# Performance work log

Measured on AMD Instinct MI355X. Metric: run time of the kernel, lower is better.

## Reference

```python
import jax, jax.numpy as jnp
import numpy as np

NUM_HEADS = 16
ROPE_BASE = 10000.0
MAX_POS = 4096


def _rope_tables(head_dim):
    inv_freq = 1.0 / (ROPE_BASE ** (np.arange(0, head_dim, 2, dtype=np.float32) / head_dim))
    freqs = np.arange(MAX_POS, dtype=np.float32)[:, None] * inv_freq[None, :]
    emb = np.concatenate([freqs, freqs], axis=-1)  # [MAX_POS, head_dim]
    return jnp.asarray(np.cos(emb)), jnp.asarray(np.sin(emb))


def _rotate_half(x):
    d = x.shape[-1] // 2
    return jnp.concatenate([-x[..., d:], x[..., :d]], axis=-1)


def _apply_rope(x, pos, cos_t, sin_t):
    # x: [B,H,S,D], pos: [B,S]
    cos = cos_t[pos][:, None]  # [B,1,S,D]
    sin = sin_t[pos][:, None]
    return x * cos + _rotate_half(x) * sin


def setup_inputs() -> dict:
    key = jax.random.key(0)
    ks = jax.random.split(key, 8)
    B, N, M, C = 2, 2048, 2048, 1024
    s = 1.0 / np.sqrt(C)
    return {
        "query": jax.random.normal(ks[0], (B, N, C), jnp.float32),
        "key": jax.random.normal(ks[1], (B, M, C), jnp.float32),
        "query_pos": jnp.broadcast_to(jnp.arange(N, dtype=jnp.int32), (B, N)),
        "key_pos": jnp.broadcast_to(jnp.arange(M, dtype=jnp.int32), (B, M)),
        "Wq": jax.random.normal(ks[2], (C, C), jnp.float32) * s,
        "bq": jnp.zeros((C,), jnp.float32),
        "Wk": jax.random.normal(ks[3], (C, C), jnp.float32) * s,
        "Wv": jax.random.normal(ks[4], (C, C), jnp.float32) * s,
        "bv": jnp.zeros((C,), jnp.float32),
        "Wo": jax.random.normal(ks[5], (C, C), jnp.float32) * s,
        "bo": jnp.zeros((C,), jnp.float32),
    }


def reference(query, key, query_pos, key_pos, Wq, bq, Wk, Wv, bv, Wo, bo):
    B, N, C = query.shape
    M = key.shape[1]
    H = NUM_HEADS
    D = C // H
    scale = D ** -0.5
    cos_t, sin_t = _rope_tables(D)

    value = key  # value defaults to key
    identity = query

    q = (query @ Wq.T + bq).reshape(B, N, H, D).transpose(0, 2, 1, 3)
    k = (key @ Wk.T).reshape(B, M, H, D).transpose(0, 2, 1, 3)
    v = (value @ Wv.T + bv).reshape(B, M, H, D).transpose(0, 2, 1, 3)

    q = _apply_rope(q, query_pos, cos_t, sin_t)
    k = _apply_rope(k, key_pos, cos_t, sin_t)

    attn = jnp.einsum('bhnd,bhmd->bhnm', q, k) * scale
    attn = jax.nn.softmax(attn, axis=-1)
    x = jnp.einsum('bhnm,bhmd->bhnd', attn, v)  # [B,H,N,D]
    x = x.transpose(0, 2, 1, 3).reshape(B, N, C)
    x = x @ Wo.T + bo
    return x + identity
```

## Files before the change

### kernel.cpp

```cpp
#include <hip/hip_runtime.h>
#include <hip/hip_bf16.h>
#include <stdint.h>

#define B_ 2
#define N_ 2048
#define M_ 2048
#define C_ 1024
#define H_ 16
#define D_ 64

typedef __attribute__((ext_vector_type(8))) short s16x8;
typedef __attribute__((ext_vector_type(4))) short s16x4;
typedef __attribute__((ext_vector_type(4))) float f32x4;
typedef __attribute__((ext_vector_type(16))) float f32x16;

__device__ __attribute__((always_inline)) inline short f2b(float f){
    __hip_bfloat16 h = __float2bfloat16(f); short s; __builtin_memcpy(&s, &h, 2); return s;
}
__device__ __attribute__((always_inline)) inline float b2f(short s){
    __hip_bfloat16 h; __builtin_memcpy(&h, &s, 2); return __bfloat162float(h);
}

#define MFMA16(a,b,c) __builtin_amdgcn_mfma_f32_16x16x32_bf16(a,b,c,0,0,0)
#define MFMA32(a,b,c) __builtin_amdgcn_mfma_f32_32x32x16_bf16(a,b,c,0,0,0)

__device__ __attribute__((always_inline)) inline void gl_lds16(const void* g, void* l){
    __builtin_amdgcn_global_load_lds((__attribute__((address_space(1))) void*)g,
                                     (__attribute__((address_space(3))) void*)l, 16, 0, 0);
}
__device__ __attribute__((always_inline)) inline unsigned fbits(float f){
    unsigned u; __builtin_memcpy(&u, &f, 4); return u;
}

__global__ void cvt_all(const float* __restrict__ q, const float* __restrict__ k,
                        const float* __restrict__ wq, const float* __restrict__ wk,
                        const float* __restrict__ wv, const float* __restrict__ wo,
                        short* __restrict__ dst){
    long i = ((long)blockIdx.x * 256 + threadIdx.x) * 8;
    const float* src; long off;
    if      (i <  4194304L){ src = q;  off = i; }
    else if (i <  8388608L){ src = k;  off = i - 4194304L; }
    else if (i <  9437184L){ src = wq; off = i - 8388608L; }
    else if (i < 10485760L){ src = wk; off = i - 9437184L; }
    else if (i < 11534336L){ src = wv; off = i - 10485760L; }
    else                   { src = wo; off = i - 11534336L; }
    float4 a = *(const float4*)(src + off);
    float4 b = *(const float4*)(src + off + 4);
    s16x8 o;
    o[0]=f2b(a.x); o[1]=f2b(a.y); o[2]=f2b(a.z); o[3]=f2b(a.w);
    o[4]=f2b(b.x); o[5]=f2b(b.y); o[6]=f2b(b.z); o[7]=f2b(b.w);
    *(s16x8*)(dst + i) = o;
}

__global__ __launch_bounds__(256, 2) void gemm_qkv(
    const short* __restrict__ qbf, const short* __restrict__ kbf,
    const short* __restrict__ W,
    const float* __restrict__ bq, const float* __restrict__ bv,
    short* __restrict__ qproj, short* __restrict__ kproj, short* __restrict__ vproj)
{
    __shared__ short As[128 * 32];
    __shared__ short Bs[128 * 32];
    const int n0 = blockIdx.x * 128, m0 = blockIdx.y * 128;
    const int sel = n0 >> 10;
    const short* A = (sel == 0) ? qbf : kbf;
    const int tid = threadIdx.x, lane = tid & 63, wave = tid >> 6;
    const int quad = lane >> 4, l16 = lane & 15;
    const int wr = (wave >> 1) * 64, wc = (wave & 1) * 64;
    const int srow = lane >> 2, scol = (lane & 3) * 8;

    f32x4 acc[4][4] = {};

    const short* Ag = A + (size_t)(m0 + wave * 32 + srow) * C_ + scol;
    const short* Bg = W + (size_t)(n0 + wave * 32 + srow) * C_ + scol;
    short* lA0 = As + (wave * 32) * 32;
    short* lA1 = As + (wave * 32 + 16) * 32;
    short* lB0 = Bs + (wave * 32) * 32;
    short* lB1 = Bs + (wave * 32 + 16) * 32;

    for (int k0 = 0; k0 < C_; k0 += 32){
        __syncthreads();
        gl_lds16(Ag + k0, lA0);
        gl_lds16(Ag + k0 + 16 * (size_t)C_, lA1);
        gl_lds16(Bg + k0, lB0);
        gl_lds16(Bg + k0 + 16 * (size_t)C_, lB1);
        __syncthreads();
        s16x8 af[4], bfr[4];
        #pragma unroll
        for (int t = 0; t < 4; t++) af[t]  = *(const s16x8*)&As[(wr + t*16 + l16) * 32 + quad * 8];
        #pragma unroll
        for (int t = 0; t < 4; t++) bfr[t] = *(const s16x8*)&Bs[(wc + t*16 + l16) * 32 + quad * 8];
        #pragma unroll
        for (int i = 0; i < 4; i++)
            #pragma unroll
            for (int j = 0; j < 4; j++)
                acc[i][j] = MFMA16(af[i], bfr[j], acc[i][j]);
    }

    short* dst = (sel == 0) ? qproj : ((sel == 1) ? kproj : vproj);
    const float* bp = (sel == 0) ? bq : ((sel == 2) ? bv : nullptr);
    const int coff = sel << 10;
    #pragma unroll
    for (int j = 0; j < 4; j++){
        int c = n0 + wc + j * 16 + l16 - coff;
        float bb = bp ? bp[c] : 0.0f;
        #pragma unroll
        for (int i = 0; i < 4; i++){
            int row = m0 + wr + i * 16 + quad * 4;
            #pragma unroll
            for (int r = 0; r < 4; r++)
                dst[(size_t)(row + r) * C_ + c] = f2b(acc[i][j][r] + bb);
        }
    }
}

__global__ __launch_bounds__(256, 2) void gemm_out(
    const short* __restrict__ A, const short* __restrict__ W,
    const float* __restrict__ bias, const float* __restrict__ resid,
    float* __restrict__ outf)
{
    __shared__ short As[128 * 32];
    __shared__ short Bs[128 * 32];
    const int n0 = blockIdx.x * 128, m0 = blockIdx.y * 128;
    const int tid = threadIdx.x, lane = tid & 63, wave = tid >> 6;
    const int quad = lane >> 4, l16 = lane & 15;
    const int wr = (wave >> 1) * 64, wc = (wave & 1) * 64;
    const int srow = lane >> 2, scol = (lane & 3) * 8;

    f32x4 acc[4][4] = {};
    const short* Ag = A + (size_t)(m0 + wave * 32 + srow) * C_ + scol;
    const short* Bg = W + (size_t)(n0 + wave * 32 + srow) * C_ + scol;
    short* lA0 = As + (wave * 32) * 32;
    short* lA1 = As + (wave * 32 + 16) * 32;
    short* lB0 = Bs + (wave * 32) * 32;
    short* lB1 = Bs + (wave * 32 + 16) * 32;

    for (int k0 = 0; k0 < C_; k0 += 32){
        __syncthreads();
        gl_lds16(Ag + k0, lA0);
        gl_lds16(Ag + k0 + 16 * (size_t)C_, lA1);
        gl_lds16(Bg + k0, lB0);
        gl_lds16(Bg + k0 + 16 * (size_t)C_, lB1);
        __syncthreads();
        s16x8 af[4], bfr[4];
        #pragma unroll
        for (int t = 0; t < 4; t++) af[t]  = *(const s16x8*)&As[(wr + t*16 + l16) * 32 + quad * 8];
        #pragma unroll
        for (int t = 0; t < 4; t++) bfr[t] = *(const s16x8*)&Bs[(wc + t*16 + l16) * 32 + quad * 8];
        #pragma unroll
        for (int i = 0; i < 4; i++)
            #pragma unroll
            for (int j = 0; j < 4; j++)
                acc[i][j] = MFMA16(af[i], bfr[j], acc[i][j]);
    }

    #pragma unroll
    for (int j = 0; j < 4; j++){
        int c = n0 + wc + j * 16 + l16;
        float bb = bias[c];
        #pragma unroll
        for (int i = 0; i < 4; i++){
            int row = m0 + wr + i * 16 + quad * 4;
            #pragma unroll
            for (int r = 0; r < 4; r++){
                size_t idx = (size_t)(row + r) * C_ + c;
                outf[idx] = acc[i][j][r] + bb + resid[idx];
            }
        }
    }
}

__global__ void rope_kernel(short* __restrict__ q, short* __restrict__ k,
                            const int* __restrict__ qpos, const int* __restrict__ kpos){
    const int QP = B_ * N_ * H_ * 32;
    int idx = blockIdx.x * blockDim.x + threadIdx.x;
    if (idx >= 2 * QP) return;
    bool isK = idx >= QP;
    int t = isK ? idx - QP : idx;
    int i = t & 31;
    int h = (t >> 5) & (H_ - 1);
    int row = t >> 9;
    int pos = isK ? kpos[row] : qpos[row];
    short* base = (isK ? k : q) + (size_t)row * C_ + h * D_;
    float x1 = b2f(base[i]), x2 = b2f(base[i + 32]);
    float invf = exp2f((float)i * (-13.287712379549449f / 32.0f));
    float f = (float)pos * invf;
    float c = cosf(f), s = sinf(f);
    float o1 = x1 * c - x2 * s;
    float o2 = x2 * c + x1 * s;
    float fac = isK ? 1.0f : (0.125f * 1.4426950408889634f);
    base[i]      = f2b(o1 * fac);
    base[i + 32] = f2b(o2 * fac);
}

__global__ void transpose_v(const short* __restrict__ v, short* __restrict__ vt){
    __shared__ short tile[64][72];
    int b = blockIdx.y >> 4, h = blockIdx.y & 15, mt = blockIdx.x;
    int tid = threadIdx.x;
    for (int c = tid; c < 512; c += 256){
        int m = c >> 3, d8 = (c & 7) * 8;
        *(s16x8*)&tile[m][d8] =
            *(const s16x8*)&v[((size_t)(b * M_ + mt * 64 + m)) * C_ + h * D_ + d8];
    }
    __syncthreads();
    for (int c = tid; c < 512; c += 256){
        int d = c >> 3, m8 = (c & 7) * 8;
        s16x8 o;
        #pragma unroll
        for (int jj = 0; jj < 8; jj++) o[jj] = tile[m8 + jj][d];
        *(s16x8*)&vt[(((size_t)(b * H_ + h)) * D_ + d) * M_ + mt * 64 + m8] = o;
    }
}

__global__ __launch_bounds__(256, 2) void flash_attn(
    const short* __restrict__ q, const short* __restrict__ k,
    const short* __restrict__ vt, short* __restrict__ o)
{
    __shared__ short smem[27136];
    const int b = blockIdx.y >> 4, h = blockIdx.y & 15;
    const int n0 = blockIdx.x * 128;
    const int tid = threadIdx.x, lane = tid & 63, wave = tid >> 6;
    const int hi = lane >> 5, l32 = lane & 31;
    const int wq = wave & 1, kq = wave >> 1;

    s16x8 qf[2][4];
    #pragma unroll
    for (int qt = 0; qt < 2; qt++)
        #pragma unroll
        for (int c = 0; c < 4; c++)
            qf[qt][c] = *(const s16x8*)&q[((size_t)(b * N_ + n0 + wq * 64 + qt * 32 + l32)) * C_
                                          + h * D_ + c * 16 + hi * 8];

    const short* kg = k  + (size_t)(b * M_) * C_ + h * D_;
    const short* vg = vt + ((size_t)(b * H_ + h)) * D_ * M_;
    const int srow0 = tid >> 3, sseg = (tid & 7) * 8;

    union V8 { s16x8 v; uint2 u[2]; };
    V8 kreg[2], vreg[2];

    #pragma unroll
    for (int ii = 0; ii < 2; ii++){
        int row = srow0 + 32 * ii;
        kreg[ii].v = *(const s16x8*)&kg[(size_t)row * C_ + sseg];
        vreg[ii].v = *(const s16x8*)&vg[(size_t)row * M_ + sseg];
    }
    #pragma unroll
    for (int ii = 0; ii < 2; ii++){
        int row = srow0 + 32 * ii;
        short* kd = &smem[row * 68 + sseg];
        *(uint2*)kd = kreg[ii].u[0]; *(uint2*)(kd + 4) = kreg[ii].u[1];
        short* vd = &smem[8704 + row * 68 + sseg];
        *(uint2*)vd = vreg[ii].u[0]; *(uint2*)(vd + 4) = vreg[ii].u[1];
    }

    f32x16 zero16 = {};
    f32x16 oacc[2][2] = {zero16, zero16, zero16, zero16};
    float lacc[2] = {0.f, 0.f};
    short* Pw = &smem[17408 + wave * 2304];

    for (int st = 0; st < 32; st++){
        const int p = st & 1;
        __syncthreads();
        if (st < 31){
            #pragma unroll
            for (int ii = 0; ii < 2; ii++){
                int row = srow0 + 32 * ii;
                kreg[ii].v = *(const s16x8*)&kg[((size_t)((st + 1) * 64 + row)) * C_ + sseg];
                vreg[ii].v = *(const s16x8*)&vg[(size_t)row * M_ + (st + 1) * 64 + sseg];
            }
        }
        const short* Kp = &smem[p * 4352];
        const short* Vp = &smem[8704 + p * 4352];

        s16x4 kf[4][2];
        #pragma unroll
        for (int c = 0; c < 4; c++){
            const short* a = &Kp[(kq * 32 + l32) * 68 + c * 16 + hi * 8];
            kf[c][0] = *(const s16x4*)a; kf[c][1] = *(const s16x4*)(a + 4);
        }
        #pragma unroll
        for (int qt = 0; qt < 2; qt++){
            f32x16 sv = {};
            #pragma unroll
            for (int c = 0; c < 4; c++){
                s16x8 ka = __builtin_shufflevector(kf[c][0], kf[c][1], 0,1,2,3,4,5,6,7);
                sv = MFMA32(ka, qf[qt][c], sv);
            }
            float ls = 0.f;
            unsigned pb[8];
            #pragma unroll
            for (int g = 0; g < 4; g++){
                float p0 = __builtin_amdgcn_exp2f(sv[4*g+0]);
                float p1 = __builtin_amdgcn_exp2f(sv[4*g+1]);
                float p2 = __builtin_amdgcn_exp2f(sv[4*g+2]);
                float p3 = __builtin_amdgcn_exp2f(sv[4*g+3]);
                ls += (p0 + p1) + (p2 + p3);
                pb[2*g]   = __builtin_amdgcn_perm(fbits(p1), fbits(p0), 0x07060302);
                pb[2*g+1] = __builtin_amdgcn_perm(fbits(p3), fbits(p2), 0x07060302);
            }
            lacc[qt] += ls;
            #pragma unroll
            for (int g = 0; g < 4; g++){
                short* d = &Pw[(qt * 32 + l32) * 36 + 8 * g + 4 * hi];
                uint2 u; u.x = pb[2*g]; u.y = pb[2*g+1];
                *(uint2*)d = u;
            }
        }
        asm volatile("s_waitcnt lgkmcnt(0)" ::: "memory");

        s16x8 pf[2][2], vf[2][2];
        #pragma unroll
        for (int qt = 0; qt < 2; qt++)
            #pragma unroll
            for (int c = 0; c < 2; c++){
                const short* a = &Pw[(qt * 32 + l32) * 36 + c * 16 + hi * 8];
                pf[qt][c] = __builtin_shufflevector(*(const s16x4*)a, *(const s16x4*)(a + 4),
                                                    0,1,2,3,4,5,6,7);
            }
        #pragma unroll
        for (int dt = 0; dt < 2; dt++)
            #pragma unroll
            for (int c = 0; c < 2; c++){
                const short* a = &Vp[(dt * 32 + l32) * 68 + kq * 32 + c * 16 + hi * 8];
                vf[dt][c] = __builtin_shufflevector(*(const s16x4*)a, *(const s16x4*)(a + 4),
                                                    0,1,2,3,4,5,6,7);
            }
        #pragma unroll
        for (int qt = 0; qt < 2; qt++)
            #pragma unroll
            for (int dt = 0; dt < 2; dt++)
                #pragma unroll
                for (int c = 0; c < 2; c++)
                    oacc[qt][dt] = MFMA32(pf[qt][c], vf[dt][c], oacc[qt][dt]);

        __syncthreads();
        if (st < 31){
            int pn = p ^ 1;
            #pragma unroll
            for (int ii = 0; ii < 2; ii++){
                int row = srow0 + 32 * ii;
                short* kd = &smem[pn * 4352 + row * 68 + sseg];
                *(uint2*)kd = kreg[ii].u[0]; *(uint2*)(kd + 4) = kreg[ii].u[1];
                short* vd = &smem[8704 + pn * 4352 + row * 68 + sseg];
                *(uint2*)vd = vreg[ii].u[0]; *(uint2*)(vd + 4) = vreg[ii].u[1];
            }
        }
    }

    __syncthreads();

    float* LO   = (float*)smem;
    float* Lsum = (float*)&smem[26624];
    float* Linv = Lsum + 128;

    float l0[2];
    #pragma unroll
    for (int qt = 0; qt < 2; qt++)
        l0[qt] = lacc[qt] + __shfl_xor(lacc[qt], 32);

    if (kq == 1){
        #pragma unroll
        for (int qt = 0; qt < 2; qt++)
            Lsum[wq * 64 + qt * 32 + l32] = l0[qt];
        #pragma unroll
        for (int qt = 0; qt < 2; qt++)
            #pragma unroll
            for (int dt = 0; dt < 2; dt++)
                #pragma unroll
                for (int e = 0; e < 16; e++){
                    int qrow = wq * 64 + qt * 32 + (e & 3) + 8 * (e >> 2) + 4 * hi;
                    LO[qrow * 65 + dt * 32 + l32] = oacc[qt][dt][e];
                }
    }
    __syncthreads();
    if (kq == 0){
        #pragma unroll
        for (int qt = 0; qt < 2; qt++){
            float lt = l0[qt] + Lsum[wq * 64 + qt * 32 + l32];
            Linv[wq * 64 + qt * 32 + l32] = 1.0f / lt;
        }
        asm volatile("s_waitcnt lgkmcnt(0)" ::: "memory");
        #pragma unroll
        for (int qt = 0; qt < 2; qt++)
            #pragma unroll
            for (int dt = 0; dt < 2; dt++)
                #pragma unroll
                for (int e = 0; e < 16; e++){
                    int qrow = wq * 64 + qt * 32 + (e & 3) + 8 * (e >> 2) + 4 * hi;
                    float val = (oacc[qt][dt][e] + LO[qrow * 65 + dt * 32 + l32]) * Linv[qrow];
                    o[((size_t)(b * N_ + n0 + qrow)) * C_ + h * D_ + dt * 32 + l32] = f2b(val);
                }
    }
}

extern "C" void kernel_launch(void* const* d_in, const int* in_sizes, int n_in,
                              void* d_out, int out_size, void* d_ws, size_t ws_size,
                              hipStream_t stream) {
    const float* query = (const float*)d_in[0];
    const float* key   = (const float*)d_in[1];
    const int*   qpos  = (const int*)d_in[2];
    const int*   kpos  = (const int*)d_in[3];
    const float* Wq    = (const float*)d_in[4];
    const float* bq    = (const float*)d_in[5];
    const float* Wk    = (const float*)d_in[6];
    const float* Wv    = (const float*)d_in[7];
    const float* bv    = (const float*)d_in[8];
    const float* Wo    = (const float*)d_in[9];
    const float* bo    = (const float*)d_in[10];
    float* out = (float*)d_out;

    const size_t E4M = (size_t)4 * 1024 * 1024;
    const size_t E1M = (size_t)1024 * 1024;
    short* ws    = (short*)d_ws;
    short* qbf   = ws;
    short* kbf   = qbf   + E4M;
    short* wqkvb = kbf   + E4M;
    short* wob   = wqkvb + 3 * E1M;
    short* qproj = wob   + E1M;
    short* kproj = qproj + E4M;
    short* vproj = kproj + E4M;
    short* vT    = qbf;
    short* attn  = kbf;

    cvt_all<<<6144, 256, 0, stream>>>(query, key, Wq, Wk, Wv, Wo, ws);

    gemm_qkv<<<dim3(24, 32), 256, 0, stream>>>(qbf, kbf, wqkvb, bq, bv,
                                               qproj, kproj, vproj);

    rope_kernel<<<(2 * B_ * N_ * H_ * 32) / 256, 256, 0, stream>>>(qproj, kproj, qpos, kpos);

    transpose_v<<<dim3(M_ / 64, B_ * H_), 256, 0, stream>>>(vproj, vT);

    flash_attn<<<dim3(16, 32), 256, 0, stream>>>(qproj, kproj, vT, attn);

    gemm_out<<<dim3(8, 32), 256, 0, stream>>>(attn, wob, bo, query, out);
}
```

Measured before the change: 235.5 us.

## Halve flash-attn and output-GEMM tiles to double block counts and raise occupancy

The flash attention kernel now handles 64 query rows per block instead of 128, doubling the grid to 1024 blocks, with a smaller shared-memory footprint and launch bounds raised to 3 blocks per CU. The output projection GEMM uses 128x64 tiles with each wave owning 32 rows, doubling its grid to 512 blocks at 4 blocks per CU. gemm_qkv's launch bound is also raised to 3. The goal is to fill the 256 CUs better than the earlier 512- and 256-block grids did. The cost is less K/V reuse per block, so more global and LDS traffic, and possible register spills under the tighter launch bounds.

```diff
diff --git a/kernel.cpp b/kernel.cpp
--- a/kernel.cpp
+++ b/kernel.cpp
@@ -52,7 +52,7 @@
     *(s16x8*)(dst + i) = o;
 }
 
-__global__ __launch_bounds__(256, 2) void gemm_qkv(
+__global__ __launch_bounds__(256, 3) void gemm_qkv(
     const short* __restrict__ qbf, const short* __restrict__ kbf,
     const short* __restrict__ W,
     const float* __restrict__ bq, const float* __restrict__ bv,
@@ -113,41 +113,39 @@
     }
 }
 
-__global__ __launch_bounds__(256, 2) void gemm_out(
+__global__ __launch_bounds__(256, 4) void gemm_out(
     const short* __restrict__ A, const short* __restrict__ W,
     const float* __restrict__ bias, const float* __restrict__ resid,
     float* __restrict__ outf)
 {
     __shared__ short As[128 * 32];
-    __shared__ short Bs[128 * 32];
-    const int n0 = blockIdx.x * 128, m0 = blockIdx.y * 128;
+    __shared__ short Bs[64 * 32];
+    const int n0 = blockIdx.x * 64, m0 = blockIdx.y * 128;
     const int tid = threadIdx.x, lane = tid & 63, wave = tid >> 6;
     const int quad = lane >> 4, l16 = lane & 15;
-    const int wr = (wave >> 1) * 64, wc = (wave & 1) * 64;
     const int srow = lane >> 2, scol = (lane & 3) * 8;
-
-    f32x4 acc[4][4] = {};
+    const int srowB = lane >> 2;
+
+    f32x4 acc[2][4] = {};
     const short* Ag = A + (size_t)(m0 + wave * 32 + srow) * C_ + scol;
-    const short* Bg = W + (size_t)(n0 + wave * 32 + srow) * C_ + scol;
+    const short* Bg = W + (size_t)(n0 + wave * 16 + srowB) * C_ + scol;
     short* lA0 = As + (wave * 32) * 32;
     short* lA1 = As + (wave * 32 + 16) * 32;
-    short* lB0 = Bs + (wave * 32) * 32;
-    short* lB1 = Bs + (wave * 32 + 16) * 32;
+    short* lB  = Bs + (wave * 16) * 32;
 
     for (int k0 = 0; k0 < C_; k0 += 32){
         __syncthreads();
         gl_lds16(Ag + k0, lA0);
         gl_lds16(Ag + k0 + 16 * (size_t)C_, lA1);
-        gl_lds16(Bg + k0, lB0);
-        gl_lds16(Bg + k0 + 16 * (size_t)C_, lB1);
-        __syncthreads();
-        s16x8 af[4], bfr[4];
-        #pragma unroll
-        for (int t = 0; t < 4; t++) af[t]  = *(const s16x8*)&As[(wr + t*16 + l16) * 32 + quad * 8];
-        #pragma unroll
-        for (int t = 0; t < 4; t++) bfr[t] = *(const s16x8*)&Bs[(wc + t*16 + l16) * 32 + quad * 8];
-        #pragma unroll
-        for (int i = 0; i < 4; i++)
+        gl_lds16(Bg + k0, lB);
+        __syncthreads();
+        s16x8 af[2], bfr[4];
+        #pragma unroll
+        for (int t = 0; t < 2; t++) af[t]  = *(const s16x8*)&As[(wave*32 + t*16 + l16) * 32 + quad * 8];
+        #pragma unroll
+        for (int t = 0; t < 4; t++) bfr[t] = *(const s16x8*)&Bs[(t*16 + l16) * 32 + quad * 8];
+        #pragma unroll
+        for (int i = 0; i < 2; i++)
             #pragma unroll
             for (int j = 0; j < 4; j++)
                 acc[i][j] = MFMA16(af[i], bfr[j], acc[i][j]);
@@ -155,11 +153,11 @@
 
     #pragma unroll
     for (int j = 0; j < 4; j++){
-        int c = n0 + wc + j * 16 + l16;
+        int c = n0 + j * 16 + l16;
         float bb = bias[c];
         #pragma unroll
-        for (int i = 0; i < 4; i++){
-            int row = m0 + wr + i * 16 + quad * 4;
+        for (int i = 0; i < 2; i++){
+            int row = m0 + wave * 32 + i * 16 + quad * 4;
             #pragma unroll
             for (int r = 0; r < 4; r++){
                 size_t idx = (size_t)(row + r) * C_ + c;
@@ -211,24 +209,22 @@
     }
 }
 
-__global__ __launch_bounds__(256, 2) void flash_attn(
+__global__ __launch_bounds__(256, 3) void flash_attn(
     const short* __restrict__ q, const short* __restrict__ k,
     const short* __restrict__ vt, short* __restrict__ o)
 {
-    __shared__ short smem[27136];
+    __shared__ short smem[22272];
     const int b = blockIdx.y >> 4, h = blockIdx.y & 15;
-    const int n0 = blockIdx.x * 128;
+    const int n0 = blockIdx.x * 64;
     const int tid = threadIdx.x, lane = tid & 63, wave = tid >> 6;
     const int hi = lane >> 5, l32 = lane & 31;
     const int wq = wave & 1, kq = wave >> 1;
 
-    s16x8 qf[2][4];
+    s16x8 qf[4];
     #pragma unroll
-    for (int qt = 0; qt < 2; qt++)
-        #pragma unroll
-        for (int c = 0; c < 4; c++)
-            qf[qt][c] = *(const s16x8*)&q[((size_t)(b * N_ + n0 + wq * 64 + qt * 32 + l32)) * C_
-                                          + h * D_ + c * 16 + hi * 8];
+    for (int c = 0; c < 4; c++)
+        qf[c] = *(const s16x8*)&q[((size_t)(b * N_ + n0 + wq * 32 + l32)) * C_
+                                  + h * D_ + c * 16 + hi * 8];
 
     const short* kg = k  + (size_t)(b * M_) * C_ + h * D_;
     const short* vg = vt + ((size_t)(b * H_ + h)) * D_ * M_;
@@ -253,9 +249,9 @@
     }
 
     f32x16 zero16 = {};
-    f32x16 oacc[2][2] = {zero16, zero16, zero16, zero16};
-    float lacc[2] = {0.f, 0.f};
-    short* Pw = &smem[17408 + wave * 2304];
+    f32x16 oacc[2] = {zero16, zero16};
+    float lacc = 0.f;
+    short* Pw = &smem[17408 + wave * 1152];
 
     for (int st = 0; st < 32; st++){
         const int p = st & 1;
@@ -277,45 +273,40 @@
             const short* a = &Kp[(kq * 32 + l32) * 68 + c * 16 + hi * 8];
             kf[c][0] = *(const s16x4*)a; kf[c][1] = *(const s16x4*)(a + 4);
         }
-        #pragma unroll
-        for (int qt = 0; qt < 2; qt++){
-            f32x16 sv = {};
-            #pragma unroll
-            for (int c = 0; c < 4; c++){
-                s16x8 ka = __builtin_shufflevector(kf[c][0], kf[c][1], 0,1,2,3,4,5,6,7);
-                sv = MFMA32(ka, qf[qt][c], sv);
-            }
-            float ls = 0.f;
-            unsigned pb[8];
-            #pragma unroll
-            for (int g = 0; g < 4; g++){
-                float p0 = __builtin_amdgcn_exp2f(sv[4*g+0]);
-                float p1 = __builtin_amdgcn_exp2f(sv[4*g+1]);
-                float p2 = __builtin_amdgcn_exp2f(sv[4*g+2]);
-                float p3 = __builtin_amdgcn_exp2f(sv[4*g+3]);
-                ls += (p0 + p1) + (p2 + p3);
-                pb[2*g]   = __builtin_amdgcn_perm(fbits(p1), fbits(p0), 0x07060302);
-                pb[2*g+1] = __builtin_amdgcn_perm(fbits(p3), fbits(p2), 0x07060302);
-            }
-            lacc[qt] += ls;
-            #pragma unroll
-            for (int g = 0; g < 4; g++){
-                short* d = &Pw[(qt * 32 + l32) * 36 + 8 * g + 4 * hi];
-                uint2 u; u.x = pb[2*g]; u.y = pb[2*g+1];
-                *(uint2*)d = u;
-            }
+        f32x16 sv = {};
+        #pragma unroll
+        for (int c = 0; c < 4; c++){
+            s16x8 ka = __builtin_shufflevector(kf[c][0], kf[c][1], 0,1,2,3,4,5,6,7);
+            sv = MFMA32(ka, qf[c], sv);
+        }
+        float ls = 0.f;
+        unsigned pb[8];
+        #pragma unroll
+        for (int g = 0; g < 4; g++){
+            float p0 = __builtin_amdgcn_exp2f(sv[4*g+0]);
+            float p1 = __builtin_amdgcn_exp2f(sv[4*g+1]);
+            float p2 = __builtin_amdgcn_exp2f(sv[4*g+2]);
+            float p3 = __builtin_amdgcn_exp2f(sv[4*g+3]);
+            ls += (p0 + p1) + (p2 + p3);
+            pb[2*g]   = __builtin_amdgcn_perm(fbits(p1), fbits(p0), 0x07060302);
+            pb[2*g+1] = __builtin_amdgcn_perm(fbits(p3), fbits(p2), 0x07060302);
+        }
+        lacc += ls;
+        #pragma unroll
+        for (int g = 0; g < 4; g++){
+            short* d = &Pw[l32 * 36 + 8 * g + 4 * hi];
+            uint2 u; u.x = pb[2*g]; u.y = pb[2*g+1];
+            *(uint2*)d = u;
         }
         asm volatile("s_waitcnt lgkmcnt(0)" ::: "memory");
 
-        s16x8 pf[2][2], vf[2][2];
-        #pragma unroll
-        for (int qt = 0; qt < 2; qt++)
-            #pragma unroll
-            for (int c = 0; c < 2; c++){
-                const short* a = &Pw[(qt * 32 + l32) * 36 + c * 16 + hi * 8];
-                pf[qt][c] = __builtin_shufflevector(*(const s16x4*)a, *(const s16x4*)(a + 4),
-                                                    0,1,2,3,4,5,6,7);
-            }
+        s16x8 pf[2], vf[2][2];
+        #pragma unroll
+        for (int c = 0; c < 2; c++){
+            const short* a = &Pw[l32 * 36 + c * 16 + hi * 8];
+            pf[c] = __builtin_shufflevector(*(const s16x4*)a, *(const s16x4*)(a + 4),
+                                            0,1,2,3,4,5,6,7);
+        }
         #pragma unroll
         for (int dt = 0; dt < 2; dt++)
             #pragma unroll
@@ -325,12 +316,10 @@
                                                     0,1,2,3,4,5,6,7);
             }
         #pragma unroll
-        for (int qt = 0; qt < 2; qt++)
-            #pragma unroll
-            for (int dt = 0; dt < 2; dt++)
-                #pragma unroll
-                for (int c = 0; c < 2; c++)
-                    oacc[qt][dt] = MFMA32(pf[qt][c], vf[dt][c], oacc[qt][dt]);
+        for (int dt = 0; dt < 2; dt++)
+            #pragma unroll
+            for (int c = 0; c < 2; c++)
+                oacc[dt] = MFMA32(pf[c], vf[dt][c], oacc[dt]);
 
         __syncthreads();
         if (st < 31){
@@ -349,46 +338,34 @@
     __syncthreads();
 
     float* LO   = (float*)smem;
-    float* Lsum = (float*)&smem[26624];
-    float* Linv = Lsum + 128;
-
-    float l0[2];
-    #pragma unroll
-    for (int qt = 0; qt < 2; qt++)
-        l0[qt] = lacc[qt] + __shfl_xor(lacc[qt], 32);
+    float* Lsum = (float*)&smem[22016];
+    float* Linv = Lsum + 64;
+
+    float l0 = lacc + __shfl_xor(lacc, 32);
 
     if (kq == 1){
-        #pragma unroll
-        for (int qt = 0; qt < 2; qt++)
-            Lsum[wq * 64 + qt * 32 + l32] = l0[qt];
-        #pragma unroll
-        for (int qt = 0; qt < 2; qt++)
-            #pragma unroll
-            for (int dt = 0; dt < 2; dt++)
-                #pragma unroll
-                for (int e = 0; e < 16; e++){
-                    int qrow = wq * 64 + qt * 32 + (e & 3) + 8 * (e >> 2) + 4 * hi;
-                    LO[qrow * 65 + dt * 32 + l32] = oacc[qt][dt][e];
-                }
+        Lsum[wq * 32 + l32] = l0;
+        #pragma unroll
+        for (int dt = 0; dt < 2; dt++)
+            #pragma unroll
+            for (int e = 0; e < 16; e++){
+                int qrow = wq * 32 + (e & 3) + 8 * (e >> 2) + 4 * hi;
+                LO[qrow * 65 + dt * 32 + l32] = oacc[dt][e];
+            }
     }
     __syncthreads();
     if (kq == 0){
-        #pragma unroll
-        for (int qt = 0; qt < 2; qt++){
-            float lt = l0[qt] + Lsum[wq * 64 + qt * 32 + l32];
-            Linv[wq * 64 + qt * 32 + l32] = 1.0f / lt;
-        }
+        float lt = l0 + Lsum[wq * 32 + l32];
+        Linv[wq * 32 + l32] = 1.0f / lt;
         asm volatile("s_waitcnt lgkmcnt(0)" ::: "memory");
         #pragma unroll
-        for (int qt = 0; qt < 2; qt++)
-            #pragma unroll
-            for (int dt = 0; dt < 2; dt++)
-                #pragma unroll
-                for (int e = 0; e < 16; e++){
-                    int qrow = wq * 64 + qt * 32 + (e & 3) + 8 * (e >> 2) + 4 * hi;
-                    float val = (oacc[qt][dt][e] + LO[qrow * 65 + dt * 32 + l32]) * Linv[qrow];
-                    o[((size_t)(b * N_ + n0 + qrow)) * C_ + h * D_ + dt * 32 + l32] = f2b(val);
-                }
+        for (int dt = 0; dt < 2; dt++)
+            #pragma unroll
+            for (int e = 0; e < 16; e++){
+                int qrow = wq * 32 + (e & 3) + 8 * (e >> 2) + 4 * hi;
+                float val = (oacc[dt][e] + LO[qrow * 65 + dt * 32 + l32]) * Linv[qrow];
+                o[((size_t)(b * N_ + n0 + qrow)) * C_ + h * D_ + dt * 32 + l32] = f2b(val);
+            }
     }
 }
 
@@ -430,7 +407,7 @@
 
     transpose_v<<<dim3(M_ / 64, B_ * H_), 256, 0, stream>>>(vproj, vT);
 
-    flash_attn<<<dim3(16, 32), 256, 0, stream>>>(qproj, kproj, vT, attn);
-
-    gemm_out<<<dim3(8, 32), 256, 0, stream>>>(attn, wob, bo, query, out);
-}
+    flash_attn<<<dim3(32, 32), 256, 0, stream>>>(qproj, kproj, vT, attn);
+
+    gemm_out<<<dim3(16, 32), 256, 0, stream>>>(attn, wob, bo, query, out);
+}
```

Result: no change. 235.4 us (-0.0%).
